# Performance work log

Hardware: AMD Instinct MI355X
Metric: run time of the kernel (lower is better)

The kernel has to match this reference:

```python
import jax, jax.numpy as jnp
import numpy as np

E = 64; H = 4; HD = 16; HID = 256; AD = 32; NS = 64
TEMP = 0.25; TOPK = 8


def rmsnorm(x, w):
    return x * jax.lax.rsqrt(jnp.mean(x * x, axis=-1, keepdims=True) + 1e-5) * w


def l2norm(x):
    n = jnp.linalg.norm(x, axis=-1, keepdims=True)
    return x / jnp.maximum(n, 1e-12)


def setup_inputs() -> dict:
    key = jax.random.key(0)
    ks = jax.random.split(key, 20)
    B, S = 32, 1024
    s = 0.02
    return {
        "x": jax.random.normal(ks[0], (B, S, E), jnp.float32),
        "memory_addresses": jax.random.normal(ks[1], (NS, AD), jnp.float32),
        "memory_values": jax.random.normal(ks[2], (B, NS, E), jnp.float32),
        "attn_norm_w": jnp.ones((E,), jnp.float32),
        "wq": jax.random.normal(ks[3], (E, E), jnp.float32) * s,
        "wk": jax.random.normal(ks[4], (E, E), jnp.float32) * s,
        "wv": jax.random.normal(ks[5], (E, E), jnp.float32) * s,
        "wo": jax.random.normal(ks[6], (E, E), jnp.float32) * s,
        "mem_norm_w": jnp.ones((E,), jnp.float32),
        "mem_q": jax.random.normal(ks[7], (AD, E), jnp.float32) * s,
        "mem_out": jax.random.normal(ks[8], (E, E), jnp.float32) * s,
        "ffn_norm_w": jnp.ones((E,), jnp.float32),
        "ffn_w1": jax.random.normal(ks[9], (HID, E), jnp.float32) * s,
        "ffn_b1": jnp.zeros((HID,), jnp.float32),
        "ffn_w2": jax.random.normal(ks[10], (E, HID), jnp.float32) * s,
        "ffn_b2": jnp.zeros((E,), jnp.float32),
    }


def decoder_block(x, memory_addresses, memory_values, attn_norm_w, wq, wk, wv, wo,
                  mem_norm_w, mem_q, mem_out, ffn_norm_w, ffn_w1, ffn_b1, ffn_w2, ffn_b2):
    B, S, _ = x.shape
    # --- causal self-attention ---
    h = rmsnorm(x, attn_norm_w)
    def heads(t):  # [B,S,E] -> [B,H,S,HD]
        return t.reshape(B, S, H, HD).transpose(0, 2, 1, 3)
    q = heads(h @ wq.T); k = heads(h @ wk.T); v = heads(h @ wv.T)
    scores = jnp.einsum("bhqd,bhkd->bhqk", q, k) / jnp.sqrt(jnp.float32(HD))
    causal = jnp.triu(jnp.ones((S, S), bool), k=1)
    scores = jnp.where(causal, -jnp.inf, scores)
    attn = jax.nn.softmax(scores, axis=-1)
    av = jnp.einsum("bhqk,bhkd->bhqd", attn, v).transpose(0, 2, 1, 3).reshape(B, S, E)
    x = x + av @ wo.T
    # --- sparse latent address read ---
    h = rmsnorm(x, mem_norm_w)
    queries = l2norm(h @ mem_q.T)                      # [B,S,AD]
    addresses = l2norm(memory_addresses)               # [NS,AD]
    read_scores = (queries @ addresses.T) / TEMP       # [B,S,NS]
    top_scores, top_idx = jax.lax.top_k(read_scores, TOPK)
    read_w = jax.nn.softmax(top_scores, axis=-1)       # [B,S,K]
    sel = memory_values[jnp.arange(B)[:, None, None], top_idx]  # [B,S,K,E]
    read_vals = jnp.einsum("bsk,bske->bse", read_w, sel)
    x = x + read_vals @ mem_out.T
    # --- feed-forward ---
    h = rmsnorm(x, ffn_norm_w)
    hid = jax.nn.gelu(h @ ffn_w1.T + ffn_b1, approximate=False)
    x = x + (hid @ ffn_w2.T + ffn_b2)
    return x


def reference(x, memory_addresses, memory_values, attn_norm_w, wq, wk, wv, wo,
              mem_norm_w, mem_q, mem_out, ffn_norm_w, ffn_w1, ffn_b1, ffn_w2, ffn_b2):
    return decoder_block(x, memory_addresses, memory_values, attn_norm_w, wq, wk, wv, wo,
                         mem_norm_w, mem_q, mem_out, ffn_norm_w, ffn_w1, ffn_b1, ffn_w2, ffn_b2)
```

## Files before the change

kernel.cpp:

```cpp
#include <hip/hip_runtime.h>
#include <hip/hip_bf16.h>
#include <math.h>

#define SEQ 1024
#define BATCH 32
#define NTOK (BATCH * SEQ)

__global__ __launch_bounds__(256) void prep_kernel(
    const float* __restrict__ maddr, const float* __restrict__ wq,
    const float* __restrict__ wk, const float* __restrict__ wv,
    const float* __restrict__ aw, const float* __restrict__ mw,
    const float* __restrict__ mq, const float* __restrict__ fw,
    const float* __restrict__ w1, const float* __restrict__ w2,
    float* __restrict__ wall, float* __restrict__ mqT, float* __restrict__ addrNT,
    float* __restrict__ w1c, float* __restrict__ w2T) {
  int gt = blockIdx.x * 256 + threadIdx.x;
  const int GS = 64 * 256;
  for (int i = gt; i < 4096; i += GS) {
    float s = aw[i & 63];
    wall[i] = wq[i] * s;
    wall[4096 + i] = wk[i] * s;
    wall[8192 + i] = wv[i] * s;
  }
  for (int i = gt; i < 2048; i += GS) {
    int e = i >> 5, a = i & 31;
    mqT[i] = mq[a * 64 + e] * mw[e];
  }
  for (int i = gt; i < 16384; i += GS) w1c[i] = w1[i] * fw[i & 63];
  for (int i = gt; i < 16384; i += GS) {
    int j = i >> 6, e = i & 63;
    w2T[i] = w2[e * 256 + j];
  }
  if (gt < 64) {
    int n = gt;
    float ss = 0.f;
    for (int a = 0; a < 32; ++a) { float t = maddr[n * 32 + a]; ss += t * t; }
    float inv = 1.0f / fmaxf(sqrtf(ss), 1e-12f);
    for (int a = 0; a < 32; ++a) addrNT[a * 64 + n] = maddr[n * 32 + a] * inv;
  }
}

__global__ __launch_bounds__(256) void qkv_kernel(
    const float* __restrict__ x, const float* __restrict__ wall,
    float* __restrict__ qkvAll) {
  __shared__ float w[12288];
  int tid = threadIdx.x;
  for (int i = tid; i < 12288; i += 256) w[i] = wall[i];
  __syncthreads();
  int token = blockIdx.x * 64 + (tid & 63);
  int p = tid >> 6;
  const float4* xr4 = (const float4*)(x + (size_t)token * 64);
  float xr[64];
#pragma unroll
  for (int c = 0; c < 16; ++c) {
    float4 t = xr4[c];
    xr[4 * c] = t.x; xr[4 * c + 1] = t.y; xr[4 * c + 2] = t.z; xr[4 * c + 3] = t.w;
  }
  float s0 = 0, s1 = 0, s2 = 0, s3 = 0;
#pragma unroll
  for (int c = 0; c < 16; ++c) {
    s0 = fmaf(xr[4 * c], xr[4 * c], s0);
    s1 = fmaf(xr[4 * c + 1], xr[4 * c + 1], s1);
    s2 = fmaf(xr[4 * c + 2], xr[4 * c + 2], s2);
    s3 = fmaf(xr[4 * c + 3], xr[4 * c + 3], s3);
  }
  float rs = rsqrtf(((s0 + s1) + (s2 + s3)) * (1.0f / 64.0f) + 1e-5f);
  const size_t BIG = (size_t)NTOK * 64;
  for (int o = 0; o < 48; ++o) {
    int idx = p * 48 + o;
    const float4* w4 = (const float4*)(w + idx * 64);
    float a0 = 0, a1 = 0, a2 = 0, a3 = 0;
#pragma unroll
    for (int c = 0; c < 16; ++c) {
      float4 ww = w4[c];
      a0 = fmaf(xr[4 * c], ww.x, a0);
      a1 = fmaf(xr[4 * c + 1], ww.y, a1);
      a2 = fmaf(xr[4 * c + 2], ww.z, a2);
      a3 = fmaf(xr[4 * c + 3], ww.w, a3);
    }
    qkvAll[(size_t)(idx >> 6) * BIG + (size_t)token * 64 + (idx & 63)] =
        ((a0 + a1) + (a2 + a3)) * rs;
  }
}

__global__ __launch_bounds__(128) void attn_kernel(
    const float* qb, const float* __restrict__ kb,
    const float* __restrict__ vb, float* avb) {
  __shared__ float kv[2 * 2048];
  int tid = threadIdx.x;
  int qt = 7 - (blockIdx.x & 7);
  int h = blockIdx.y, b = blockIdx.z;
  int qi = qt * 128 + tid;
  size_t base = (size_t)b * SEQ * 64 + h * 16;
  float qv[16];
  {
    const float4* qr = (const float4*)(qb + base + (size_t)qi * 64);
#pragma unroll
    for (int c = 0; c < 4; ++c) {
      float4 t = qr[c];
      qv[4 * c] = t.x; qv[4 * c + 1] = t.y; qv[4 * c + 2] = t.z; qv[4 * c + 3] = t.w;
    }
  }
  int wavebase = __builtin_amdgcn_readfirstlane(qi);
  int myNT = (wavebase >> 6) + 1;
  int nt = 2 * qt + 2;
  int kj = tid >> 1, part = tid & 1;
  const float* src0 = (part ? vb : kb) + base;
  float m = -1e30f, l = 0.f;
  float o[16];
#pragma unroll
  for (int d = 0; d < 16; ++d) o[d] = 0.f;
  float4 pA, pB, pC, pD;
  {
    const float4* s4 = (const float4*)(src0 + (size_t)kj * 64);
    pA = s4[0]; pB = s4[1]; pC = s4[2]; pD = s4[3];
  }
  for (int jt = 0; jt < nt; ++jt) {
    int buf = jt & 1;
    {
      float4* d4 = (float4*)(&kv[buf * 2048 + tid * 16]);
      d4[0] = pA; d4[1] = pB; d4[2] = pC; d4[3] = pD;
    }
    __syncthreads();
    if (jt + 1 < nt) {
      const float4* s4 = (const float4*)(src0 + (size_t)((jt + 1) * 64 + kj) * 64);
      pA = s4[0]; pB = s4[1]; pC = s4[2]; pD = s4[3];
    }
    if (jt < myNT) {
      const float* kvb = &kv[buf * 2048];
      bool diag = (jt == myNT - 1);
      for (int cc = 0; cc < 2; ++cc) {
        int cb = jt * 64 + cc * 32;
        float s[32];
#pragma unroll
        for (int u = 0; u < 32; ++u) {
          const float4* kr = (const float4*)(kvb + (cc * 32 + u) * 32);
          float4 k0 = kr[0], k1 = kr[1], k2 = kr[2], k3 = kr[3];
          float a0 = qv[0] * k0.x + qv[1] * k0.y + qv[2] * k0.z + qv[3] * k0.w;
          float a1 = qv[4] * k1.x + qv[5] * k1.y + qv[6] * k1.z + qv[7] * k1.w;
          float a2 = qv[8] * k2.x + qv[9] * k2.y + qv[10] * k2.z + qv[11] * k2.w;
          float a3 = qv[12] * k3.x + qv[13] * k3.y + qv[14] * k3.z + qv[15] * k3.w;
          s[u] = ((a0 + a1) + (a2 + a3)) * 0.25f;
        }
        if (diag) {
#pragma unroll
          for (int u = 0; u < 32; ++u) s[u] = (cb + u <= qi) ? s[u] : -1e30f;
        }
        float t0 = s[0], t1 = s[1], t2 = s[2], t3 = s[3];
#pragma unroll
        for (int u = 4; u < 32; u += 4) {
          t0 = fmaxf(t0, s[u]); t1 = fmaxf(t1, s[u + 1]);
          t2 = fmaxf(t2, s[u + 2]); t3 = fmaxf(t3, s[u + 3]);
        }
        float tm = fmaxf(fmaxf(t0, t1), fmaxf(t2, t3));
        float mn = fmaxf(m, tm);
        float cor = __expf(m - mn);
        m = mn;
        l *= cor;
#pragma unroll
        for (int d = 0; d < 16; ++d) o[d] *= cor;
        float l0 = 0, l1 = 0, l2 = 0, l3 = 0;
#pragma unroll
        for (int u = 0; u < 32; u += 4) {
          float p0 = __expf(s[u] - m);     s[u] = p0;     l0 += p0;
          float p1 = __expf(s[u + 1] - m); s[u + 1] = p1; l1 += p1;
          float p2 = __expf(s[u + 2] - m); s[u + 2] = p2; l2 += p2;
          float p3 = __expf(s[u + 3] - m); s[u + 3] = p3; l3 += p3;
        }
        l += (l0 + l1) + (l2 + l3);
#pragma unroll
        for (int u = 0; u < 32; ++u) {
          const float4* vr = (const float4*)(kvb + (cc * 32 + u) * 32 + 16);
          float4 v0 = vr[0], v1 = vr[1], v2 = vr[2], v3 = vr[3];
          float pu = s[u];
          o[0] = fmaf(pu, v0.x, o[0]);   o[1] = fmaf(pu, v0.y, o[1]);
          o[2] = fmaf(pu, v0.z, o[2]);   o[3] = fmaf(pu, v0.w, o[3]);
          o[4] = fmaf(pu, v1.x, o[4]);   o[5] = fmaf(pu, v1.y, o[5]);
          o[6] = fmaf(pu, v1.z, o[6]);   o[7] = fmaf(pu, v1.w, o[7]);
          o[8] = fmaf(pu, v2.x, o[8]);   o[9] = fmaf(pu, v2.y, o[9]);
          o[10] = fmaf(pu, v2.z, o[10]); o[11] = fmaf(pu, v2.w, o[11]);
          o[12] = fmaf(pu, v3.x, o[12]); o[13] = fmaf(pu, v3.y, o[13]);
          o[14] = fmaf(pu, v3.z, o[14]); o[15] = fmaf(pu, v3.w, o[15]);
        }
      }
    }
    __syncthreads();
  }
  float inv = 1.0f / l;
  float4* outp = (float4*)(avb + base + (size_t)qi * 64);
#pragma unroll
  for (int c = 0; c < 4; ++c) {
    float4 t;
    t.x = o[4 * c] * inv; t.y = o[4 * c + 1] * inv;
    t.z = o[4 * c + 2] * inv; t.w = o[4 * c + 3] * inv;
    outp[c] = t;
  }
}

__global__ __launch_bounds__(256) void womem_a_kernel(
    const float* __restrict__ x, const float* avb,
    const float* __restrict__ wo, float* __restrict__ x1b) {
  __shared__ float wos[4096];
  int tid = threadIdx.x;
  for (int i = tid; i < 4096; i += 256) wos[i] = wo[i];
  __syncthreads();
  int token = blockIdx.x * 64 + (tid & 63);
  int p = tid >> 6;
  float av[64];
  {
    const float4* a4 = (const float4*)(avb + (size_t)token * 64);
#pragma unroll
    for (int c = 0; c < 16; ++c) {
      float4 t = a4[c];
      av[4 * c] = t.x; av[4 * c + 1] = t.y; av[4 * c + 2] = t.z; av[4 * c + 3] = t.w;
    }
  }
  for (int o = 0; o < 16; ++o) {
    int r = p * 16 + o;
    const float4* wr = (const float4*)(wos + r * 64);
    float a0 = 0, a1 = 0, a2 = 0, a3 = 0;
#pragma unroll
    for (int c = 0; c < 16; ++c) {
      float4 w4 = wr[c];
      a0 = fmaf(av[4 * c], w4.x, a0);
      a1 = fmaf(av[4 * c + 1], w4.y, a1);
      a2 = fmaf(av[4 * c + 2], w4.z, a2);
      a3 = fmaf(av[4 * c + 3], w4.w, a3);
    }
    x1b[(size_t)token * 64 + r] = x[(size_t)token * 64 + r] + ((a0 + a1) + (a2 + a3));
  }
}

__global__ __launch_bounds__(64) void womem_b_kernel(
    const float* __restrict__ x1b, const float* __restrict__ mqT,
    const float* __restrict__ addrNT, const float* __restrict__ mo,
    const float* __restrict__ mv, float* __restrict__ x2b) {
  __shared__ float mqs[2048];
  __shared__ float ads[2048];
  __shared__ float mos[4096];
  __shared__ float scr[64 * 65];
  __shared__ float tval[64 * 9];
  __shared__ int   tidxs[64 * 9];
  int tid = threadIdx.x;
  for (int i = tid; i < 2048; i += 64) { mqs[i] = mqT[i]; ads[i] = addrNT[i]; }
  for (int i = tid; i < 4096; i += 64) mos[i] = mo[i];
  __syncthreads();
  int token = blockIdx.x * 64 + tid;
  int b = token >> 10;
  const float4* x14 = (const float4*)(x1b + (size_t)token * 64);
  float q[32];
#pragma unroll
  for (int a = 0; a < 32; ++a) q[a] = 0.f;
  for (int e4 = 0; e4 < 16; ++e4) {
    float4 xv = x14[e4];
    float tc[4] = {xv.x, xv.y, xv.z, xv.w};
#pragma unroll
    for (int ec = 0; ec < 4; ++ec) {
      float t = tc[ec];
      const float4* mq4 = (const float4*)(mqs + (e4 * 4 + ec) * 32);
#pragma unroll
      for (int a4 = 0; a4 < 8; ++a4) {
        float4 mm = mq4[a4];
        q[4 * a4]     = fmaf(t, mm.x, q[4 * a4]);
        q[4 * a4 + 1] = fmaf(t, mm.y, q[4 * a4 + 1]);
        q[4 * a4 + 2] = fmaf(t, mm.z, q[4 * a4 + 2]);
        q[4 * a4 + 3] = fmaf(t, mm.w, q[4 * a4 + 3]);
      }
    }
  }
  float qq = 0.f;
#pragma unroll
  for (int a = 0; a < 32; ++a) qq = fmaf(q[a], q[a], qq);
  float sinv = 4.0f / fmaxf(sqrtf(qq), 1e-12f);
  for (int n4 = 0; n4 < 16; ++n4) {
    float a0 = 0, a1 = 0, a2 = 0, a3 = 0;
#pragma unroll
    for (int a = 0; a < 32; ++a) {
      float4 an = *(const float4*)(ads + a * 64 + n4 * 4);
      a0 = fmaf(q[a], an.x, a0);
      a1 = fmaf(q[a], an.y, a1);
      a2 = fmaf(q[a], an.z, a2);
      a3 = fmaf(q[a], an.w, a3);
    }
    scr[tid * 65 + n4 * 4]     = a0 * sinv;
    scr[tid * 65 + n4 * 4 + 1] = a1 * sinv;
    scr[tid * 65 + n4 * 4 + 2] = a2 * sinv;
    scr[tid * 65 + n4 * 4 + 3] = a3 * sinv;
  }
  for (int kk = 0; kk < 8; ++kk) {
    float bv = -1e30f; int bi = 0;
    for (int n = 0; n < 64; ++n) {
      float v = scr[tid * 65 + n];
      if (v > bv) { bv = v; bi = n; }
    }
    tval[tid * 9 + kk] = bv;
    tidxs[tid * 9 + kk] = bi;
    scr[tid * 65 + bi] = -3e30f;
  }
  float vmax = tval[tid * 9];
  float psum = 0.f;
  for (int kk = 0; kk < 8; ++kk) {
    float pw = __expf(tval[tid * 9 + kk] - vmax);
    tval[tid * 9 + kk] = pw;
    psum += pw;
  }
  float isum = 1.0f / psum;
  float rv[64];
#pragma unroll
  for (int e = 0; e < 64; ++e) rv[e] = 0.f;
  for (int kk = 0; kk < 8; ++kk) {
    float wgt = tval[tid * 9 + kk] * isum;
    int ix = tidxs[tid * 9 + kk];
    const float4* mr = (const float4*)(mv + ((size_t)(b * 64 + ix)) * 64);
#pragma unroll
    for (int c = 0; c < 16; ++c) {
      float4 f = mr[c];
      rv[4 * c]     = fmaf(wgt, f.x, rv[4 * c]);
      rv[4 * c + 1] = fmaf(wgt, f.y, rv[4 * c + 1]);
      rv[4 * c + 2] = fmaf(wgt, f.z, rv[4 * c + 2]);
      rv[4 * c + 3] = fmaf(wgt, f.w, rv[4 * c + 3]);
    }
  }
  float4* out4 = (float4*)(x2b + (size_t)token * 64);
  for (int e4 = 0; e4 < 16; ++e4) {
    float4 xv = x14[e4];
    float res[4];
#pragma unroll
    for (int ec = 0; ec < 4; ++ec) {
      const float4* mr = (const float4*)(mos + (e4 * 4 + ec) * 64);
      float a0 = 0, a1 = 0, a2 = 0, a3 = 0;
#pragma unroll
      for (int c = 0; c < 16; ++c) {
        float4 w4 = mr[c];
        a0 = fmaf(rv[4 * c], w4.x, a0);
        a1 = fmaf(rv[4 * c + 1], w4.y, a1);
        a2 = fmaf(rv[4 * c + 2], w4.z, a2);
        a3 = fmaf(rv[4 * c + 3], w4.w, a3);
      }
      res[ec] = ((a0 + a1) + (a2 + a3));
    }
    float4 t;
    t.x = xv.x + res[0]; t.y = xv.y + res[1];
    t.z = xv.z + res[2]; t.w = xv.w + res[3];
    out4[e4] = t;
  }
}

__global__ __launch_bounds__(256) void ffn1_kernel(
    const float* __restrict__ x2b, const float* __restrict__ w1c,
    const float* __restrict__ b1, __hip_bfloat16* __restrict__ hidT) {
  __shared__ float w1s[128 * 64];
  int tid = threadIdx.x;
  int chunk = blockIdx.y;
  for (int i = tid; i < 8192; i += 256) w1s[i] = w1c[chunk * 8192 + i];
  __syncthreads();
  int token = blockIdx.x * 64 + (tid & 63);
  int p = tid >> 6;
  const float4* x4 = (const float4*)(x2b + (size_t)token * 64);
  float xr[64];
#pragma unroll
  for (int c = 0; c < 16; ++c) {
    float4 t = x4[c];
    xr[4 * c] = t.x; xr[4 * c + 1] = t.y; xr[4 * c + 2] = t.z; xr[4 * c + 3] = t.w;
  }
  float s0 = 0, s1 = 0, s2 = 0, s3 = 0;
#pragma unroll
  for (int c = 0; c < 16; ++c) {
    s0 = fmaf(xr[4 * c], xr[4 * c], s0);
    s1 = fmaf(xr[4 * c + 1], xr[4 * c + 1], s1);
    s2 = fmaf(xr[4 * c + 2], xr[4 * c + 2], s2);
    s3 = fmaf(xr[4 * c + 3], xr[4 * c + 3], s3);
  }
  float rs = rsqrtf(((s0 + s1) + (s2 + s3)) * (1.0f / 64.0f) + 1e-5f);
  for (int o = 0; o < 32; ++o) {
    int rl = p * 32 + o;
    int rg = chunk * 128 + rl;
    const float4* wr = (const float4*)(w1s + rl * 64);
    float a0 = 0, a1 = 0, a2 = 0, a3 = 0;
#pragma unroll
    for (int c = 0; c < 16; ++c) {
      float4 w4 = wr[c];
      a0 = fmaf(xr[4 * c], w4.x, a0);
      a1 = fmaf(xr[4 * c + 1], w4.y, a1);
      a2 = fmaf(xr[4 * c + 2], w4.z, a2);
      a3 = fmaf(xr[4 * c + 3], w4.w, a3);
    }
    float hv = ((a0 + a1) + (a2 + a3)) * rs + b1[rg];
    float g = 0.5f * hv * (1.0f + erff(hv * 0.70710678118654752f));
    hidT[(size_t)rg * NTOK + token] = __float2bfloat16(g);
  }
}

__global__ __launch_bounds__(256) void ffn2_kernel(
    const float* __restrict__ x2b, const __hip_bfloat16* __restrict__ hidT,
    const float* __restrict__ w2T, const float* __restrict__ b2,
    float* __restrict__ out) {
  __shared__ float w2s[128 * 64];
  __shared__ float acc[64 * 65];
  int tid = threadIdx.x;
  int token = blockIdx.x * 64 + (tid & 63);
  int p = tid >> 6;
  int lrow = tid & 63;
  for (int i = tid; i < 64 * 65; i += 256) acc[i] = 0.f;
  float part[64];
#pragma unroll
  for (int e = 0; e < 64; ++e) part[e] = 0.f;
  for (int c = 0; c < 2; ++c) {
    __syncthreads();
    for (int i = tid; i < 8192; i += 256) w2s[i] = w2T[c * 8192 + i];
    __syncthreads();
    for (int jo = 0; jo < 32; ++jo) {
      int jl = p * 32 + jo;
      int j = c * 128 + jl;
      float hv = __bfloat162float(hidT[(size_t)j * NTOK + token]);
      const float4* wr = (const float4*)(w2s + jl * 64);
#pragma unroll
      for (int cc = 0; cc < 16; ++cc) {
        float4 w4 = wr[cc];
        part[4 * cc]     = fmaf(hv, w4.x, part[4 * cc]);
        part[4 * cc + 1] = fmaf(hv, w4.y, part[4 * cc + 1]);
        part[4 * cc + 2] = fmaf(hv, w4.z, part[4 * cc + 2]);
        part[4 * cc + 3] = fmaf(hv, w4.w, part[4 * cc + 3]);
      }
    }
  }
  __syncthreads();
#pragma unroll
  for (int e = 0; e < 64; ++e) atomicAdd(&acc[lrow * 65 + e], part[e]);
  __syncthreads();
  int e0 = p * 16;
#pragma unroll
  for (int i = 0; i < 16; ++i) {
    int e = e0 + i;
    out[(size_t)token * 64 + e] = x2b[(size_t)token * 64 + e] + b2[e] + acc[lrow * 65 + e];
  }
}

extern "C" void kernel_launch(void* const* d_in, const int* in_sizes, int n_in,
                              void* d_out, int out_size, void* d_ws, size_t ws_size,
                              hipStream_t stream) {
  const float* x    = (const float*)d_in[0];
  const float* addr = (const float*)d_in[1];
  const float* mv   = (const float*)d_in[2];
  const float* aw   = (const float*)d_in[3];
  const float* wq   = (const float*)d_in[4];
  const float* wk   = (const float*)d_in[5];
  const float* wv   = (const float*)d_in[6];
  const float* wo   = (const float*)d_in[7];
  const float* mw   = (const float*)d_in[8];
  const float* mq   = (const float*)d_in[9];
  const float* mo   = (const float*)d_in[10];
  const float* fw   = (const float*)d_in[11];
  const float* w1   = (const float*)d_in[12];
  const float* b1   = (const float*)d_in[13];
  const float* w2   = (const float*)d_in[14];
  const float* b2   = (const float*)d_in[15];

  float* ws = (float*)d_ws;
  const size_t BIG = (size_t)NTOK * 64;
  float* qb  = ws;
  float* kb  = ws + BIG;
  float* vb  = ws + 2 * BIG;
  float* avb = qb;
  float* x1b = kb;
  float* x2b = vb;
  __hip_bfloat16* hidT = (__hip_bfloat16*)d_ws;
  float* sm = ws + 3 * BIG;
  float* wall   = sm;
  float* mqT    = sm + 12288;
  float* addrNT = sm + 14336;
  float* w1c    = sm + 16384;
  float* w2T    = sm + 32768;

  prep_kernel<<<64, 256, 0, stream>>>(addr, wq, wk, wv, aw, mw, mq, fw, w1, w2,
                                      wall, mqT, addrNT, w1c, w2T);
  qkv_kernel<<<512, 256, 0, stream>>>(x, wall, qb);
  attn_kernel<<<dim3(8, 4, BATCH), 128, 0, stream>>>(qb, kb, vb, avb);
  womem_a_kernel<<<512, 256, 0, stream>>>(x, avb, wo, x1b);
  womem_b_kernel<<<512, 64, 0, stream>>>(x1b, mqT, addrNT, mo, mv, x2b);
  ffn1_kernel<<<dim3(512, 2), 256, 0, stream>>>(x2b, w1c, b1, hidT);
  ffn2_kernel<<<512, 256, 0, stream>>>(x2b, hidT, w2T, b2, (float*)d_out);
}
```

Before: 508.1 us.

## Split attention key range across four waves per query tile and merge partial softmax

```diff
diff --git a/kernel.cpp b/kernel.cpp
--- a/kernel.cpp
+++ b/kernel.cpp
@@ -83,14 +83,16 @@
   }
 }
 
-__global__ __launch_bounds__(128) void attn_kernel(
+__global__ __launch_bounds__(512) void attn_kernel(
     const float* qb, const float* __restrict__ kb,
     const float* __restrict__ vb, float* avb) {
-  __shared__ float kv[2 * 2048];
-  int tid = threadIdx.x;
-  int qt = 7 - (blockIdx.x & 7);
+  __shared__ float smem[9728];
+  int tid = threadIdx.x;
+  int w = tid >> 6, lane = tid & 63;
+  int ks = w >> 1, half = w & 1;
+  int qt = 7 - blockIdx.x;
   int h = blockIdx.y, b = blockIdx.z;
-  int qi = qt * 128 + tid;
+  int qi = qt * 128 + half * 64 + lane;
   size_t base = (size_t)b * SEQ * 64 + h * 16;
   float qv[16];
   {
@@ -101,99 +103,112 @@
       qv[4 * c] = t.x; qv[4 * c + 1] = t.y; qv[4 * c + 2] = t.z; qv[4 * c + 3] = t.w;
     }
   }
-  int wavebase = __builtin_amdgcn_readfirstlane(qi);
-  int myNT = (wavebase >> 6) + 1;
-  int nt = 2 * qt + 2;
-  int kj = tid >> 1, part = tid & 1;
+  int nt = qt + 1;
+  int key0w = ks * nt * 32;
+  int kj = lane >> 1, part = lane & 1;
   const float* src0 = (part ? vb : kb) + base;
+  float* kvw = smem + w * 1152;
   float m = -1e30f, l = 0.f;
   float o[16];
 #pragma unroll
   for (int d = 0; d < 16; ++d) o[d] = 0.f;
   float4 pA, pB, pC, pD;
   {
-    const float4* s4 = (const float4*)(src0 + (size_t)kj * 64);
+    const float4* s4 = (const float4*)(src0 + (size_t)(key0w + kj) * 64);
     pA = s4[0]; pB = s4[1]; pC = s4[2]; pD = s4[3];
   }
-  for (int jt = 0; jt < nt; ++jt) {
-    int buf = jt & 1;
+  for (int t = 0; t < nt; ++t) {
+    asm volatile("s_waitcnt lgkmcnt(0)" ::: "memory");
     {
-      float4* d4 = (float4*)(&kv[buf * 2048 + tid * 16]);
+      float4* d4 = (float4*)(kvw + kj * 36 + part * 16);
       d4[0] = pA; d4[1] = pB; d4[2] = pC; d4[3] = pD;
     }
-    __syncthreads();
-    if (jt + 1 < nt) {
-      const float4* s4 = (const float4*)(src0 + (size_t)((jt + 1) * 64 + kj) * 64);
+    asm volatile("s_waitcnt lgkmcnt(0)" ::: "memory");
+    __builtin_amdgcn_sched_barrier(0);
+    if (t + 1 < nt) {
+      const float4* s4 = (const float4*)(src0 + (size_t)(key0w + (t + 1) * 32 + kj) * 64);
       pA = s4[0]; pB = s4[1]; pC = s4[2]; pD = s4[3];
     }
-    if (jt < myNT) {
-      const float* kvb = &kv[buf * 2048];
-      bool diag = (jt == myNT - 1);
-      for (int cc = 0; cc < 2; ++cc) {
-        int cb = jt * 64 + cc * 32;
-        float s[32];
-#pragma unroll
-        for (int u = 0; u < 32; ++u) {
-          const float4* kr = (const float4*)(kvb + (cc * 32 + u) * 32);
-          float4 k0 = kr[0], k1 = kr[1], k2 = kr[2], k3 = kr[3];
-          float a0 = qv[0] * k0.x + qv[1] * k0.y + qv[2] * k0.z + qv[3] * k0.w;
-          float a1 = qv[4] * k1.x + qv[5] * k1.y + qv[6] * k1.z + qv[7] * k1.w;
-          float a2 = qv[8] * k2.x + qv[9] * k2.y + qv[10] * k2.z + qv[11] * k2.w;
-          float a3 = qv[12] * k3.x + qv[13] * k3.y + qv[14] * k3.z + qv[15] * k3.w;
-          s[u] = ((a0 + a1) + (a2 + a3)) * 0.25f;
-        }
-        if (diag) {
-#pragma unroll
-          for (int u = 0; u < 32; ++u) s[u] = (cb + u <= qi) ? s[u] : -1e30f;
-        }
-        float t0 = s[0], t1 = s[1], t2 = s[2], t3 = s[3];
-#pragma unroll
-        for (int u = 4; u < 32; u += 4) {
-          t0 = fmaxf(t0, s[u]); t1 = fmaxf(t1, s[u + 1]);
-          t2 = fmaxf(t2, s[u + 2]); t3 = fmaxf(t3, s[u + 3]);
-        }
-        float tm = fmaxf(fmaxf(t0, t1), fmaxf(t2, t3));
-        float mn = fmaxf(m, tm);
-        float cor = __expf(m - mn);
-        m = mn;
-        l *= cor;
-#pragma unroll
-        for (int d = 0; d < 16; ++d) o[d] *= cor;
-        float l0 = 0, l1 = 0, l2 = 0, l3 = 0;
-#pragma unroll
-        for (int u = 0; u < 32; u += 4) {
-          float p0 = __expf(s[u] - m);     s[u] = p0;     l0 += p0;
-          float p1 = __expf(s[u + 1] - m); s[u + 1] = p1; l1 += p1;
-          float p2 = __expf(s[u + 2] - m); s[u + 2] = p2; l2 += p2;
-          float p3 = __expf(s[u + 3] - m); s[u + 3] = p3; l3 += p3;
-        }
-        l += (l0 + l1) + (l2 + l3);
-#pragma unroll
-        for (int u = 0; u < 32; ++u) {
-          const float4* vr = (const float4*)(kvb + (cc * 32 + u) * 32 + 16);
-          float4 v0 = vr[0], v1 = vr[1], v2 = vr[2], v3 = vr[3];
-          float pu = s[u];
-          o[0] = fmaf(pu, v0.x, o[0]);   o[1] = fmaf(pu, v0.y, o[1]);
-          o[2] = fmaf(pu, v0.z, o[2]);   o[3] = fmaf(pu, v0.w, o[3]);
-          o[4] = fmaf(pu, v1.x, o[4]);   o[5] = fmaf(pu, v1.y, o[5]);
-          o[6] = fmaf(pu, v1.z, o[6]);   o[7] = fmaf(pu, v1.w, o[7]);
-          o[8] = fmaf(pu, v2.x, o[8]);   o[9] = fmaf(pu, v2.y, o[9]);
-          o[10] = fmaf(pu, v2.z, o[10]); o[11] = fmaf(pu, v2.w, o[11]);
-          o[12] = fmaf(pu, v3.x, o[12]); o[13] = fmaf(pu, v3.y, o[13]);
-          o[14] = fmaf(pu, v3.z, o[14]); o[15] = fmaf(pu, v3.w, o[15]);
-        }
-      }
-    }
-    __syncthreads();
-  }
-  float inv = 1.0f / l;
-  float4* outp = (float4*)(avb + base + (size_t)qi * 64);
-#pragma unroll
-  for (int c = 0; c < 4; ++c) {
-    float4 t;
-    t.x = o[4 * c] * inv; t.y = o[4 * c + 1] * inv;
-    t.z = o[4 * c + 2] * inv; t.w = o[4 * c + 3] * inv;
-    outp[c] = t;
+    int cb = key0w + t * 32;
+    float s[32];
+#pragma unroll
+    for (int u = 0; u < 32; ++u) {
+      const float4* kr = (const float4*)(kvw + u * 36);
+      float4 k0 = kr[0], k1 = kr[1], k2 = kr[2], k3 = kr[3];
+      float a0 = qv[0] * k0.x + qv[1] * k0.y + qv[2] * k0.z + qv[3] * k0.w;
+      float a1 = qv[4] * k1.x + qv[5] * k1.y + qv[6] * k1.z + qv[7] * k1.w;
+      float a2 = qv[8] * k2.x + qv[9] * k2.y + qv[10] * k2.z + qv[11] * k2.w;
+      float a3 = qv[12] * k3.x + qv[13] * k3.y + qv[14] * k3.z + qv[15] * k3.w;
+      float sc = ((a0 + a1) + (a2 + a3)) * 0.25f;
+      s[u] = (cb + u <= qi) ? sc : -1e30f;
+    }
+    float t0 = s[0], t1 = s[1], t2 = s[2], t3 = s[3];
+#pragma unroll
+    for (int u = 4; u < 32; u += 4) {
+      t0 = fmaxf(t0, s[u]); t1 = fmaxf(t1, s[u + 1]);
+      t2 = fmaxf(t2, s[u + 2]); t3 = fmaxf(t3, s[u + 3]);
+    }
+    float tm = fmaxf(fmaxf(t0, t1), fmaxf(t2, t3));
+    float mn = fmaxf(m, tm);
+    float cor = __expf(m - mn);
+    m = mn;
+    l *= cor;
+#pragma unroll
+    for (int d = 0; d < 16; ++d) o[d] *= cor;
+    float l0 = 0, l1 = 0, l2 = 0, l3 = 0;
+#pragma unroll
+    for (int u = 0; u < 32; u += 4) {
+      float p0 = __expf(s[u] - m);     s[u] = p0;     l0 += p0;
+      float p1 = __expf(s[u + 1] - m); s[u + 1] = p1; l1 += p1;
+      float p2 = __expf(s[u + 2] - m); s[u + 2] = p2; l2 += p2;
+      float p3 = __expf(s[u + 3] - m); s[u + 3] = p3; l3 += p3;
+    }
+    l += (l0 + l1) + (l2 + l3);
+#pragma unroll
+    for (int u = 0; u < 32; ++u) {
+      const float4* vr = (const float4*)(kvw + u * 36 + 16);
+      float4 v0 = vr[0], v1 = vr[1], v2 = vr[2], v3 = vr[3];
+      float pu = s[u];
+      o[0] = fmaf(pu, v0.x, o[0]);   o[1] = fmaf(pu, v0.y, o[1]);
+      o[2] = fmaf(pu, v0.z, o[2]);   o[3] = fmaf(pu, v0.w, o[3]);
+      o[4] = fmaf(pu, v1.x, o[4]);   o[5] = fmaf(pu, v1.y, o[5]);
+      o[6] = fmaf(pu, v1.z, o[6]);   o[7] = fmaf(pu, v1.w, o[7]);
+      o[8] = fmaf(pu, v2.x, o[8]);   o[9] = fmaf(pu, v2.y, o[9]);
+      o[10] = fmaf(pu, v2.z, o[10]); o[11] = fmaf(pu, v2.w, o[11]);
+      o[12] = fmaf(pu, v3.x, o[12]); o[13] = fmaf(pu, v3.y, o[13]);
+      o[14] = fmaf(pu, v3.z, o[14]); o[15] = fmaf(pu, v3.w, o[15]);
+    }
+  }
+  __syncthreads();
+  {
+    int q = half * 64 + lane;
+    float* slot = smem + (size_t)(q * 4 + ks) * 19;
+#pragma unroll
+    for (int d = 0; d < 16; ++d) slot[d] = o[d];
+    slot[16] = m; slot[17] = l;
+  }
+  __syncthreads();
+  if (tid < 128) {
+    const float* s0 = smem + (size_t)(tid * 4 + 0) * 19;
+    const float* s1 = smem + (size_t)(tid * 4 + 1) * 19;
+    const float* s2 = smem + (size_t)(tid * 4 + 2) * 19;
+    const float* s3 = smem + (size_t)(tid * 4 + 3) * 19;
+    float m0 = s0[16], m1 = s1[16], m2 = s2[16], m3 = s3[16];
+    float M = fmaxf(fmaxf(m0, m1), fmaxf(m2, m3));
+    float w0 = __expf(m0 - M), w1 = __expf(m1 - M);
+    float w2 = __expf(m2 - M), w3 = __expf(m3 - M);
+    float L = s0[17] * w0 + s1[17] * w1 + s2[17] * w2 + s3[17] * w3;
+    float inv = 1.0f / L;
+    float4* outp = (float4*)(avb + base + (size_t)(qt * 128 + tid) * 64);
+#pragma unroll
+    for (int c = 0; c < 4; ++c) {
+      float4 t4;
+      t4.x = (s0[4 * c]     * w0 + s1[4 * c]     * w1 + s2[4 * c]     * w2 + s3[4 * c]     * w3) * inv;
+      t4.y = (s0[4 * c + 1] * w0 + s1[4 * c + 1] * w1 + s2[4 * c + 1] * w2 + s3[4 * c + 1] * w3) * inv;
+      t4.z = (s0[4 * c + 2] * w0 + s1[4 * c + 2] * w1 + s2[4 * c + 2] * w2 + s3[4 * c + 2] * w3) * inv;
+      t4.w = (s0[4 * c + 3] * w0 + s1[4 * c + 3] * w1 + s2[4 * c + 3] * w2 + s3[4 * c + 3] * w3) * inv;
+      outp[c] = t4;
+    }
   }
 }
 
@@ -475,7 +490,7 @@
   prep_kernel<<<64, 256, 0, stream>>>(addr, wq, wk, wv, aw, mw, mq, fw, w1, w2,
                                       wall, mqT, addrNT, w1c, w2T);
   qkv_kernel<<<512, 256, 0, stream>>>(x, wall, qb);
-  attn_kernel<<<dim3(8, 4, BATCH), 128, 0, stream>>>(qb, kb, vb, avb);
+  attn_kernel<<<dim3(8, 4, BATCH), 512, 0, stream>>>(qb, kb, vb, avb);
   womem_a_kernel<<<512, 256, 0, stream>>>(x, avb, wo, x1b);
   womem_b_kernel<<<512, 64, 0, stream>>>(x1b, mqT, addrNT, mo, mv, x2b);
   ffn1_kernel<<<dim3(512, 2), 256, 0, stream>>>(x2b, w1c, b1, hidT);
```

Result: slower. 542.3 us (+6.7%).
